# Performance work log

Measured on AMD Instinct MI355X. Metric: run time of the kernel, lower is better.

Reference implementation:

```python
import jax, jax.numpy as jnp
import numpy as np

B, D, T, K = 32, 64, 4096, 512
COMMITMENT_COST = 0.25


def setup_inputs() -> dict:
    key = jax.random.key(0)
    k1, k2 = jax.random.split(key)
    z = jax.random.normal(k1, (B, D, T), dtype=jnp.float32)
    # nn.Embedding init: uniform(-1/K, 1/K)
    codebook = jax.random.uniform(k2, (K, D), dtype=jnp.float32,
                                  minval=-1.0 / K, maxval=1.0 / K)
    return {"z": z, "codebook": codebook}


def reference(z, codebook):
    sg = jax.lax.stop_gradient
    zt = jnp.transpose(z, (0, 2, 1))            # [B, T, D]
    zf = zt.reshape(-1, D)                      # [N, D], N = B*T
    # squared L2 distances: ||z||^2 + ||e||^2 - 2 z.e  -> [N, K]
    dists = (jnp.sum(zf * zf, axis=1, keepdims=True)
             + jnp.sum(codebook * codebook, axis=1)
             - 2.0 * jnp.matmul(zf, codebook.T))
    idx = jnp.argmin(dists, axis=1)             # [N]
    # gather codebook rows (same math as one-hot @ codebook)
    quantized = codebook[idx].reshape(zt.shape)  # [B, T, D]
    codebook_loss = jnp.mean((sg(quantized) - zt) ** 2)
    commitment_loss = jnp.mean((quantized - sg(zt)) ** 2)
    vq_loss = codebook_loss + COMMITMENT_COST * commitment_loss
    # straight-through estimator
    quantized_st = zt + sg(quantized - zt)
    quantized_out = jnp.transpose(quantized_st, (0, 2, 1))  # [B, D, T]
    indices = idx.reshape(B, T)
    return vq_loss, quantized_out, indices
```

## Files before the change

kernel.cpp:

```cpp
#include <hip/hip_runtime.h>

#define NB 32
#define ND 64
#define NT 4096
#define NK 512
#define NGRID 1024

typedef __attribute__((ext_vector_type(8))) short short8;
typedef __attribute__((ext_vector_type(16))) float f32x16;
typedef unsigned int uint32;
typedef unsigned short ushort16_t;

#define PERM(r) ((((r) & 7) * 16) + ((r) >> 3))
#define STR 68
#define ESTR 66
#define M2 2.5e-4f
#define RCAP 4

__device__ __forceinline__ ushort16_t bf16rne(float f) {
    uint32 u = __float_as_uint(f);
    return (ushort16_t)((u + 0x7FFFu + ((u >> 16) & 1u)) >> 16);
}
__device__ __forceinline__ float bf16tof(ushort16_t h) {
    return __uint_as_float(((uint32)h) << 16);
}

__global__ void prep_kernel(const float* __restrict__ cb,
                            uint4* __restrict__ cbfrag,
                            float* __restrict__ enorm,
                            double* __restrict__ loss_acc,
                            uint32* __restrict__ counter) {
    const int bi = blockIdx.x, tid = threadIdx.x;
    if (bi < 16) {
        const int t = bi * 256 + tid;
        const int c = t >> 8, rem = t & 255, s = rem >> 6, L = rem & 63;
        const int kcode = c * 32 + (L & 31);
        const int dbase = s * 16 + ((L >> 5) << 3);
        const float* src = cb + (size_t)kcode * 64 + dbase;
        const float4 pa = *(const float4*)src;
        const float4 pb = *(const float4*)(src + 4);
        const float f[8] = {pa.x, pa.y, pa.z, pa.w, pb.x, pb.y, pb.z, pb.w};
        uint32 hw[4], lw[4];
#pragma unroll
        for (int i = 0; i < 4; ++i) {
            const ushort16_t h0 = bf16rne(f[2*i]);
            const ushort16_t h1 = bf16rne(f[2*i+1]);
            const ushort16_t l0 = bf16rne(f[2*i]   - bf16tof(h0));
            const ushort16_t l1 = bf16rne(f[2*i+1] - bf16tof(h1));
            hw[i] = (uint32)h0 | ((uint32)h1 << 16);
            lw[i] = (uint32)l0 | ((uint32)l1 << 16);
        }
        cbfrag[(size_t)((c*4+s)*2 + 0)*64 + L] = make_uint4(hw[0],hw[1],hw[2],hw[3]);
        cbfrag[(size_t)((c*4+s)*2 + 1)*64 + L] = make_uint4(lw[0],lw[1],lw[2],lw[3]);
    } else {
        if (tid == 0) { *loss_acc = 0.0; *counter = 0u; }
        for (int k = tid; k < NK; k += 256) {
            const float* e = cb + (size_t)k * ND;
            float r[8];
#pragma unroll
            for (int j = 0; j < 8; ++j) {
                float s = __fmul_rn(e[j], e[j]);
#pragma unroll
                for (int i = 1; i < 8; ++i)
                    s = __fadd_rn(s, __fmul_rn(e[8*i+j], e[8*i+j]));
                r[j] = s;
            }
            enorm[k] = __fadd_rn(__fadd_rn(__fadd_rn(r[0],r[1]), __fadd_rn(r[2],r[3])),
                                 __fadd_rn(__fadd_rn(r[4],r[5]), __fadd_rn(r[6],r[7])));
        }
    }
}

__device__ __forceinline__ float exact_dist(const float* __restrict__ zrow,
                                            const float* __restrict__ cb,
                                            const float* __restrict__ enl,
                                            float zn, int k2) {
    const float4* e4 = (const float4*)(cb + (size_t)k2 * ND);
    float a = 0.0f;
#pragma unroll
    for (int w = 0; w < 16; ++w) {
        const float4 ev = e4[w];
        const float4 zv = *(const float4*)(zrow + 4 * w);
        a = __builtin_fmaf(zv.x, ev.x, a);
        a = __builtin_fmaf(zv.y, ev.y, a);
        a = __builtin_fmaf(zv.z, ev.z, a);
        a = __builtin_fmaf(zv.w, ev.w, a);
    }
    return __fsub_rn(__fadd_rn(zn, enl[k2]), __fmul_rn(2.0f, a));
}

__global__ __launch_bounds__(256, 3) void vq_main(const float* __restrict__ z,
                                                  const float* __restrict__ cb,
                                                  const uint4* __restrict__ cbfrag,
                                                  const float* __restrict__ enorm,
                                                  float* __restrict__ qout,
                                                  float* __restrict__ idxout,
                                                  double* __restrict__ loss_acc,
                                                  uint32* __restrict__ counter,
                                                  float* __restrict__ out0) {
    __shared__ __align__(16) char smem[39968];
    float*       zl   = (float*)smem;
    float*       enl  = (float*)(smem + 34816);
    float*       znl  = (float*)(smem + 36864);
    ushort16_t*  cand = (ushort16_t*)(smem + 37376);
    int*         sfin = (int*)(smem + 39424);
    double*      sred = (double*)(smem + 39936);

    const int bi    = blockIdx.x;
    const int b     = bi >> 5;
    const int tbase = (bi & 31) * 128;
    const int tid   = threadIdx.x;
    const size_t zoff = (size_t)b * (ND * NT) + tbase;

#pragma unroll
    for (int j = 0; j < 8; ++j) {
        const int qq = j * 256 + tid;
        const int i4 = qq & 31, d = qq >> 5;
        const float4 v = *(const float4*)(z + zoff + (size_t)d * NT + i4 * 4);
        const float vv[4] = {v.x, v.y, v.z, v.w};
#pragma unroll
        for (int c = 0; c < 4; ++c) {
            const int r = i4 * 4 + c;
            zl[PERM(r) * STR + d] = vv[c];
        }
    }
    for (int k = tid; k < NK; k += 256) enl[k] = enorm[k];
    __syncthreads();

    if (tid < 128) {
        const int r = tid;
        const float4* zr4 = (const float4*)&zl[PERM(r) * STR];
        float x[64];
#pragma unroll
        for (int wq = 0; wq < 16; ++wq) {
            const float4 t4 = zr4[wq];
            x[4*wq] = t4.x; x[4*wq+1] = t4.y; x[4*wq+2] = t4.z; x[4*wq+3] = t4.w;
        }
        float r8[8];
#pragma unroll
        for (int jj = 0; jj < 8; ++jj) {
            float s = __fmul_rn(x[jj], x[jj]);
#pragma unroll
            for (int ii = 1; ii < 8; ++ii)
                s = __fadd_rn(s, __fmul_rn(x[8*ii+jj], x[8*ii+jj]));
            r8[jj] = s;
        }
        znl[r] = __fadd_rn(__fadd_rn(__fadd_rn(r8[0],r8[1]), __fadd_rn(r8[2],r8[3])),
                           __fadd_rn(__fadd_rn(r8[4],r8[5]), __fadd_rn(r8[6],r8[7])));
    }

    const int L    = tid & 63;
    const int w    = tid >> 6;
    const int h    = L >> 5;
    const int rowl = w * 32 + (L & 31);
    short8 bhf[4], blf[4];
    {
        const float* zrow = &zl[PERM(rowl) * STR];
#pragma unroll
        for (int s = 0; s < 4; ++s) {
            const int d0 = s * 16 + h * 8;
            const float4 pa = *(const float4*)(zrow + d0);
            const float4 pb = *(const float4*)(zrow + d0 + 4);
            const float f[8] = {pa.x, pa.y, pa.z, pa.w, pb.x, pb.y, pb.z, pb.w};
            uint32 hw[4], lw[4];
#pragma unroll
            for (int i = 0; i < 4; ++i) {
                const ushort16_t h0 = bf16rne(f[2*i]);
                const ushort16_t h1 = bf16rne(f[2*i+1]);
                const ushort16_t l0 = bf16rne(f[2*i]   - bf16tof(h0));
                const ushort16_t l1 = bf16rne(f[2*i+1] - bf16tof(h1));
                hw[i] = (uint32)h0 | ((uint32)h1 << 16);
                lw[i] = (uint32)l0 | ((uint32)l1 << 16);
            }
            union { uint4 u; short8 s8; } uh, ul;
            uh.u = make_uint4(hw[0],hw[1],hw[2],hw[3]);
            ul.u = make_uint4(lw[0],lw[1],lw[2],lw[3]);
            bhf[s] = uh.s8; blf[s] = ul.s8;
        }
    }
    __syncthreads();

    const int h4 = h * 4;

    uint32 p1 = 0u, p2 = 0u, p3 = 0u;
#pragma unroll 2
    for (int c = 0; c < 16; ++c) {
        uint4 B[8];
#pragma unroll
        for (int p = 0; p < 8; ++p) B[p] = cbfrag[(size_t)((c * 8 + p) * 64) + L];
        f32x16 acc;
#pragma unroll
        for (int r = 0; r < 16; ++r) acc[r] = 0.0f;
#pragma unroll
        for (int s = 0; s < 4; ++s) {
            union { uint4 u; short8 s8; } ah, al;
            ah.u = B[s * 2 + 0];
            al.u = B[s * 2 + 1];
            acc = __builtin_amdgcn_mfma_f32_32x32x16_bf16(ah.s8, bhf[s], acc, 0, 0, 0);
            acc = __builtin_amdgcn_mfma_f32_32x32x16_bf16(al.s8, bhf[s], acc, 0, 0, 0);
            acc = __builtin_amdgcn_mfma_f32_32x32x16_bf16(ah.s8, blf[s], acc, 0, 0, 0);
        }
#pragma unroll
        for (int r = 0; r < 16; ++r) {
            const int kc = c * 32 + ((r & 3) + 8 * (r >> 2)) + h4;
            const uint32 pv = (__float_as_uint(fmaxf(acc[r] + 1.0f, 0.0f)) & ~0x1FFu)
                            | (uint32)kc;
            const bool g1 = pv > p1, g2 = pv > p2, g3 = pv > p3;
            p3 = g2 ? p2 : (g3 ? pv : p3);
            p2 = g1 ? p1 : (g2 ? pv : p2);
            p1 = g1 ? pv : p1;
        }
    }

    const uint32 op1 = __shfl_xor(p1, 32);
    const uint32 pkG = (p1 > op1) ? p1 : op1;
    const int    kG  = (int)(pkG & 0x1FFu);
    {
    }
    const float  bm   = __uint_as_float(pkG & ~0x1FFu) - 1.0f;
    const float  thrf = bm - M2;
    const uint32 thrF = __float_as_uint(fmaxf(thrf + 1.0f, 0.0f)) & ~0x1FFu;

    const float* zrow = &zl[PERM(rowl) * STR];
    const float  zn   = znl[rowl];
    const int    iown = (((kG >> 2) & 1) == h);

    int bkf;
    if (__any((int)(p3 >= thrF))) {
        int myc = 0, ovf = 0;
        ushort16_t* mylist = cand + (rowl * 2 + h) * RCAP;
#pragma unroll 1
        for (int c = 0; c < 16; ++c) {
            uint4 B[8];
#pragma unroll
            for (int p = 0; p < 8; ++p) B[p] = cbfrag[(size_t)((c * 8 + p) * 64) + L];
            f32x16 acc;
#pragma unroll
            for (int r = 0; r < 16; ++r) acc[r] = 0.0f;
#pragma unroll
            for (int s = 0; s < 4; ++s) {
                union { uint4 u; short8 s8; } ah, al;
                ah.u = B[s * 2 + 0];
                al.u = B[s * 2 + 1];
                acc = __builtin_amdgcn_mfma_f32_32x32x16_bf16(ah.s8, bhf[s], acc, 0, 0, 0);
                acc = __builtin_amdgcn_mfma_f32_32x32x16_bf16(al.s8, bhf[s], acc, 0, 0, 0);
                acc = __builtin_amdgcn_mfma_f32_32x32x16_bf16(ah.s8, blf[s], acc, 0, 0, 0);
            }
#pragma unroll
            for (int r = 0; r < 16; ++r) {
                const int kc = c * 32 + ((r & 3) + 8 * (r >> 2)) + h4;
                const uint32 pv = (__float_as_uint(fmaxf(acc[r] + 1.0f, 0.0f)) & ~0x1FFu)
                                | (uint32)kc;
                if (pv >= thrF && kc != kG) {
                    if (myc < RCAP) mylist[myc++] = (ushort16_t)kc;
                    else ovf = 1;
                }
            }
        }
        const int totr = myc + __shfl_xor(myc, 32);
        const int aovf = ovf | __shfl_xor(ovf, 32);
        if (aovf) {
            float bd = __builtin_inff(); bkf = 0x7FFFFFFF;
            for (int c = 0; c < 16; ++c)
#pragma unroll
                for (int qd = 0; qd < 4; ++qd)
#pragma unroll
                    for (int i = 0; i < 4; ++i) {
                        const int k2c = c * 32 + qd * 8 + h * 4 + i;
                        const float dv = exact_dist(zrow, cb, enl, zn, k2c);
                        if (dv < bd || (dv == bd && k2c < bkf)) { bd = dv; bkf = k2c; }
                    }
            const float obd = __shfl_xor(bd, 32);
            const int   obq = __shfl_xor(bkf, 32);
            if (obd < bd || (obd == bd && obq < bkf)) bkf = obq;
        } else if (totr > 0) {
            float bd = __builtin_inff(); bkf = 0x7FFFFFFF;
            if (iown) { bd = exact_dist(zrow, cb, enl, zn, kG); bkf = kG; }
            for (int i = 0; i < myc; ++i) {
                const int k2c = mylist[i];
                const float dv = exact_dist(zrow, cb, enl, zn, k2c);
                if (dv < bd || (dv == bd && k2c < bkf)) { bd = dv; bkf = k2c; }
            }
            const float obd = __shfl_xor(bd, 32);
            const int   obq = __shfl_xor(bkf, 32);
            if (obd < bd || (obd == bd && obq < bkf)) bkf = obq;
        } else {
            bkf = kG;
        }
    } else {
        const int k1 = (int)(p1 & 0x1FFu);
        const int k2 = (int)(p2 & 0x1FFu);
        const int r1v = (!iown) && (p1 >= thrF);
        const int r2v = (p2 >= thrF);
        const int nr  = r1v + r2v;
        const int totr = nr + __shfl_xor(nr, 32);
        if (totr > 0) {
            float bd = __builtin_inff(); bkf = 0x7FFFFFFF;
            if (iown) { bd = exact_dist(zrow, cb, enl, zn, kG); bkf = kG; }
            if (r1v) {
                const float dv = exact_dist(zrow, cb, enl, zn, k1);
                if (dv < bd || (dv == bd && k1 < bkf)) { bd = dv; bkf = k1; }
            }
            if (r2v) {
                const float dv = exact_dist(zrow, cb, enl, zn, k2);
                if (dv < bd || (dv == bd && k2 < bkf)) { bd = dv; bkf = k2; }
            }
            const float obd = __shfl_xor(bd, 32);
            const int   obq = __shfl_xor(bkf, 32);
            if (obd < bd || (obd == bd && obq < bkf)) bkf = obq;
        } else {
            bkf = kG;
        }
    }

    if (h == 0) {
        sfin[rowl] = bkf;
        idxout[(size_t)b * NT + tbase + rowl] = (float)bkf;
    }
    __syncthreads();

    float* ech = zl;
#pragma unroll
    for (int j = 0; j < 8; ++j) {
        const int qq  = j * 256 + tid;
        const int row = qq >> 4, d4 = qq & 15;
        const float4 v = *(const float4*)(cb + (size_t)sfin[row] * ND + d4 * 4);
        float* dst = &ech[row * ESTR + d4 * 4];
        *(float2*)(dst)     = make_float2(v.x, v.y);
        *(float2*)(dst + 2) = make_float2(v.z, v.w);
    }
    __syncthreads();

    double lsum = 0.0;
#pragma unroll 4
    for (int j = 0; j < 32; ++j) {
        const int qq = j * 256 + tid;
        const int ir = qq & 127, d = qq >> 7;
        const float zv = z[zoff + (size_t)d * NT + ir];
        const float ev = ech[ir * ESTR + d];
        const float diff = __fsub_rn(ev, zv);
        qout[(size_t)b * (ND*NT) + (size_t)d * NT + tbase + ir] = __fadd_rn(zv, diff);
        lsum += (double)diff * (double)diff;
    }
#pragma unroll
    for (int off = 32; off > 0; off >>= 1) lsum += __shfl_down(lsum, off, 64);
    if ((tid & 63) == 0) sred[tid >> 6] = lsum;
    __syncthreads();

    if (tid == 0) {
        const double bsum = (sred[0] + sred[1]) + (sred[2] + sred[3]);
        atomicAdd(loss_acc, bsum);
        __threadfence();
        const uint32 old = atomicAdd(counter, 1u);
        if (old == (uint32)(NGRID - 1)) {
            __threadfence();
            const double tot = *(volatile double*)loss_acc;
            const double m = tot / (double)((size_t)NB * NT * ND);
            out0[0] = (float)(1.25 * m);
        }
    }
}

extern "C" void kernel_launch(void* const* d_in, const int* in_sizes, int n_in,
                              void* d_out, int out_size, void* d_ws, size_t ws_size,
                              hipStream_t stream) {
    const float* z  = (const float*)d_in[0];
    const float* cb = (const float*)d_in[1];

    float* out      = (float*)d_out;
    float* loss_out = out;
    float* qout     = out + 1;
    float* idxout   = out + 1 + (size_t)NB * ND * NT;

    uint4*  cbfrag   = (uint4*)d_ws;
    float*  enorm    = (float*)((char*)d_ws + 139264);
    double* loss_acc = (double*)((char*)d_ws + 141312);
    uint32* counter  = (uint32*)((char*)d_ws + 141320);

    prep_kernel<<<17, 256, 0, stream>>>(cb, cbfrag, enorm, loss_acc, counter);
    vq_main<<<NGRID, 256, 0, stream>>>(z, cb, cbfrag, enorm, qout, idxout,
                                       loss_acc, counter, loss_out);
}
```

Before: 187.4 us.

## Split MFMA accumulators, vectorize output loop, and spread loss atomics

```diff
diff --git a/kernel.cpp b/kernel.cpp
--- a/kernel.cpp
+++ b/kernel.cpp
@@ -16,6 +16,7 @@
 #define ESTR 66
 #define M2 2.5e-4f
 #define RCAP 4
+#define NSLOT 16
 
 __device__ __forceinline__ ushort16_t bf16rne(float f) {
     uint32 u = __float_as_uint(f);
@@ -53,7 +54,8 @@
         cbfrag[(size_t)((c*4+s)*2 + 0)*64 + L] = make_uint4(hw[0],hw[1],hw[2],hw[3]);
         cbfrag[(size_t)((c*4+s)*2 + 1)*64 + L] = make_uint4(lw[0],lw[1],lw[2],lw[3]);
     } else {
-        if (tid == 0) { *loss_acc = 0.0; *counter = 0u; }
+        if (tid < NSLOT) loss_acc[tid] = 0.0;
+        if (tid == 0) *counter = 0u;
         for (int k = tid; k < NK; k += 256) {
             const float* e = cb + (size_t)k * ND;
             float r[8];
@@ -188,22 +190,23 @@
         uint4 B[8];
 #pragma unroll
         for (int p = 0; p < 8; ++p) B[p] = cbfrag[(size_t)((c * 8 + p) * 64) + L];
-        f32x16 acc;
-#pragma unroll
-        for (int r = 0; r < 16; ++r) acc[r] = 0.0f;
+        f32x16 acc0, acc1;
+#pragma unroll
+        for (int r = 0; r < 16; ++r) { acc0[r] = 0.0f; acc1[r] = 0.0f; }
 #pragma unroll
         for (int s = 0; s < 4; ++s) {
             union { uint4 u; short8 s8; } ah, al;
             ah.u = B[s * 2 + 0];
             al.u = B[s * 2 + 1];
-            acc = __builtin_amdgcn_mfma_f32_32x32x16_bf16(ah.s8, bhf[s], acc, 0, 0, 0);
-            acc = __builtin_amdgcn_mfma_f32_32x32x16_bf16(al.s8, bhf[s], acc, 0, 0, 0);
-            acc = __builtin_amdgcn_mfma_f32_32x32x16_bf16(ah.s8, blf[s], acc, 0, 0, 0);
+            acc0 = __builtin_amdgcn_mfma_f32_32x32x16_bf16(ah.s8, bhf[s], acc0, 0, 0, 0);
+            acc0 = __builtin_amdgcn_mfma_f32_32x32x16_bf16(al.s8, bhf[s], acc0, 0, 0, 0);
+            acc1 = __builtin_amdgcn_mfma_f32_32x32x16_bf16(ah.s8, blf[s], acc1, 0, 0, 0);
         }
 #pragma unroll
         for (int r = 0; r < 16; ++r) {
             const int kc = c * 32 + ((r & 3) + 8 * (r >> 2)) + h4;
-            const uint32 pv = (__float_as_uint(fmaxf(acc[r] + 1.0f, 0.0f)) & ~0x1FFu)
+            const float a = acc0[r] + acc1[r];
+            const uint32 pv = (__float_as_uint(fmaxf(a + 1.0f, 0.0f)) & ~0x1FFu)
                             | (uint32)kc;
             const bool g1 = pv > p1, g2 = pv > p2, g3 = pv > p3;
             p3 = g2 ? p2 : (g3 ? pv : p3);
@@ -215,8 +218,6 @@
     const uint32 op1 = __shfl_xor(p1, 32);
     const uint32 pkG = (p1 > op1) ? p1 : op1;
     const int    kG  = (int)(pkG & 0x1FFu);
-    {
-    }
     const float  bm   = __uint_as_float(pkG & ~0x1FFu) - 1.0f;
     const float  thrf = bm - M2;
     const uint32 thrF = __float_as_uint(fmaxf(thrf + 1.0f, 0.0f)) & ~0x1FFu;
@@ -234,22 +235,23 @@
             uint4 B[8];
 #pragma unroll
             for (int p = 0; p < 8; ++p) B[p] = cbfrag[(size_t)((c * 8 + p) * 64) + L];
-            f32x16 acc;
-#pragma unroll
-            for (int r = 0; r < 16; ++r) acc[r] = 0.0f;
+            f32x16 acc0, acc1;
+#pragma unroll
+            for (int r = 0; r < 16; ++r) { acc0[r] = 0.0f; acc1[r] = 0.0f; }
 #pragma unroll
             for (int s = 0; s < 4; ++s) {
                 union { uint4 u; short8 s8; } ah, al;
                 ah.u = B[s * 2 + 0];
                 al.u = B[s * 2 + 1];
-                acc = __builtin_amdgcn_mfma_f32_32x32x16_bf16(ah.s8, bhf[s], acc, 0, 0, 0);
-                acc = __builtin_amdgcn_mfma_f32_32x32x16_bf16(al.s8, bhf[s], acc, 0, 0, 0);
-                acc = __builtin_amdgcn_mfma_f32_32x32x16_bf16(ah.s8, blf[s], acc, 0, 0, 0);
+                acc0 = __builtin_amdgcn_mfma_f32_32x32x16_bf16(ah.s8, bhf[s], acc0, 0, 0, 0);
+                acc0 = __builtin_amdgcn_mfma_f32_32x32x16_bf16(al.s8, bhf[s], acc0, 0, 0, 0);
+                acc1 = __builtin_amdgcn_mfma_f32_32x32x16_bf16(ah.s8, blf[s], acc1, 0, 0, 0);
             }
 #pragma unroll
             for (int r = 0; r < 16; ++r) {
                 const int kc = c * 32 + ((r & 3) + 8 * (r >> 2)) + h4;
-                const uint32 pv = (__float_as_uint(fmaxf(acc[r] + 1.0f, 0.0f)) & ~0x1FFu)
+                const float a = acc0[r] + acc1[r];
+                const uint32 pv = (__float_as_uint(fmaxf(a + 1.0f, 0.0f)) & ~0x1FFu)
                                 | (uint32)kc;
                 if (pv >= thrF && kc != kG) {
                     if (myc < RCAP) mylist[myc++] = (ushort16_t)kc;
@@ -333,14 +335,21 @@
 
     double lsum = 0.0;
 #pragma unroll 4
-    for (int j = 0; j < 32; ++j) {
-        const int qq = j * 256 + tid;
-        const int ir = qq & 127, d = qq >> 7;
-        const float zv = z[zoff + (size_t)d * NT + ir];
-        const float ev = ech[ir * ESTR + d];
-        const float diff = __fsub_rn(ev, zv);
-        qout[(size_t)b * (ND*NT) + (size_t)d * NT + tbase + ir] = __fadd_rn(zv, diff);
-        lsum += (double)diff * (double)diff;
+    for (int j = 0; j < 8; ++j) {
+        const int qq  = j * 256 + tid;
+        const int ir0 = (qq & 31) * 4, d = qq >> 5;
+        const float4 zv4 = *(const float4*)(z + zoff + (size_t)d * NT + ir0);
+        const float zv[4] = {zv4.x, zv4.y, zv4.z, zv4.w};
+        float qo[4];
+#pragma unroll
+        for (int m = 0; m < 4; ++m) {
+            const float ev = ech[(ir0 + m) * ESTR + d];
+            const float diff = __fsub_rn(ev, zv[m]);
+            qo[m] = __fadd_rn(zv[m], diff);
+            lsum += (double)diff * (double)diff;
+        }
+        *(float4*)(qout + (size_t)b * (ND*NT) + (size_t)d * NT + tbase + ir0) =
+            make_float4(qo[0], qo[1], qo[2], qo[3]);
     }
 #pragma unroll
     for (int off = 32; off > 0; off >>= 1) lsum += __shfl_down(lsum, off, 64);
@@ -349,12 +358,14 @@
 
     if (tid == 0) {
         const double bsum = (sred[0] + sred[1]) + (sred[2] + sred[3]);
-        atomicAdd(loss_acc, bsum);
+        atomicAdd(loss_acc + (bi & (NSLOT - 1)), bsum);
         __threadfence();
         const uint32 old = atomicAdd(counter, 1u);
         if (old == (uint32)(NGRID - 1)) {
             __threadfence();
-            const double tot = *(volatile double*)loss_acc;
+            double tot = 0.0;
+            for (int i = 0; i < NSLOT; ++i)
+                tot += ((volatile double*)loss_acc)[i];
             const double m = tot / (double)((size_t)NB * NT * ND);
             out0[0] = (float)(1.25 * m);
         }
@@ -375,7 +386,7 @@
     uint4*  cbfrag   = (uint4*)d_ws;
     float*  enorm    = (float*)((char*)d_ws + 139264);
     double* loss_acc = (double*)((char*)d_ws + 141312);
-    uint32* counter  = (uint32*)((char*)d_ws + 141320);
+    uint32* counter  = (uint32*)((char*)d_ws + 141440);
 
     prep_kernel<<<17, 256, 0, stream>>>(cb, cbfrag, enorm, loss_acc, counter);
     vq_main<<<NGRID, 256, 0, stream>>>(z, cb, cbfrag, enorm, qout, idxout,
```

Result: faster. 178.9 us (-4.5%).
